# Kernel tuning notes

Measured on AMD Instinct MI355X. Metric: run time of the kernel, lower is better.

Reference implementation:

```python
import jax, jax.numpy as jnp
import numpy as np

EPS = 1e-5
S_CENTERS = 1024  # npoint//4
NSAMPLE = 32


def index_points(pts, idx):
    # pts [B,N,C], idx [B,...] int -> [B,...,C]
    return jax.vmap(lambda p, i: p[i])(pts, idx)


def farthest_point_sample(xyz, npoint):
    # xyz [B,N,3] -> [B,npoint] indices (deterministic start at index 0)
    B, N, _ = xyz.shape
    def body(carry, _):
        dist, far = carry
        centroid = jnp.take_along_axis(xyz, far[:, None, None], axis=1)  # [B,1,3]
        d = jnp.sum((xyz - centroid) ** 2, axis=-1)                      # [B,N]
        dist = jnp.minimum(dist, d)
        nxt = jnp.argmax(dist, axis=-1).astype(jnp.int32)
        return (dist, nxt), far
    init = (jnp.full((B, N), 1e10, xyz.dtype), jnp.zeros((B,), jnp.int32))
    _, idx = jax.lax.scan(body, init, None, length=npoint)
    return jnp.transpose(idx)  # [B,npoint]


def knn_point(k, xyz, new_xyz):
    # squared dists [B,S,N], take k nearest
    d = (jnp.sum(new_xyz ** 2, -1)[:, :, None]
         + jnp.sum(xyz ** 2, -1)[:, None, :]
         - 2.0 * jnp.einsum('bsc,bnc->bsn', new_xyz, xyz))
    _, idx = jax.lax.top_k(-d, k)
    return idx  # [B,S,k]


def instance_norm(h):
    # h [B,S,K,C]: InstanceNorm2d (affine=False) normalizes per (b,c) over spatial dims
    mu = jnp.mean(h, axis=(1, 2), keepdims=True)
    var = jnp.var(h, axis=(1, 2), keepdims=True)
    return (h - mu) * jax.lax.rsqrt(var + EPS)


def setup_inputs() -> dict:
    key = jax.random.key(0)
    ks = jax.random.split(key, 12)
    B, N, C = 8, 4096, 128
    inp = {
        'pc1_l_loc2': jax.random.normal(ks[0], (B, 3, N), jnp.float32),
        'corr_feats': jax.random.normal(ks[1], (B, C, N), jnp.float32),
        'W1': jax.random.normal(ks[2], (128, 131), jnp.float32) * 0.05,
        'b1': jnp.zeros((128,), jnp.float32),
        'W2': jax.random.normal(ks[3], (128, 128), jnp.float32) * 0.05,
        'b2': jnp.zeros((128,), jnp.float32),
        'W3': jax.random.normal(ks[4], (128, 128), jnp.float32) * 0.05,
        'b3': jnp.zeros((128,), jnp.float32),
        'fc_w': jax.random.normal(ks[5], (3, 128), jnp.float32) * 0.05,
        'fc_b': jnp.zeros((3,), jnp.float32),
    }
    return inp


def reference(pc1_l_loc2, corr_feats, W1, b1, W2, b2, W3, b3, fc_w, fc_b):
    xyz = jnp.transpose(pc1_l_loc2, (0, 2, 1))    # [B,N,3]
    points = jnp.transpose(corr_feats, (0, 2, 1))  # [B,N,128]

    fps_idx = farthest_point_sample(xyz, S_CENTERS)           # [B,S]
    new_xyz = index_points(xyz, fps_idx)                      # [B,S,3]
    idx = knn_point(NSAMPLE, xyz, new_xyz)                    # [B,S,K]
    grouped_xyz = index_points(xyz, idx)                      # [B,S,K,3]
    grouped_xyz_norm = grouped_xyz - new_xyz[:, :, None, :]
    grouped_pts = index_points(points, idx)                   # [B,S,K,128]
    h = jnp.concatenate([grouped_xyz_norm, grouped_pts], -1)  # [B,S,K,131]

    for W, b in ((W1, b1), (W2, b2), (W3, b3)):
        h = jnp.einsum('bskc,oc->bsko', h, W) + b  # 1x1 conv as matmul
        h = jax.nn.relu(instance_norm(h))

    x = jnp.max(h, axis=2)                         # [B,S,128] max over neighbors
    x = jnp.einsum('bsc,oc->bso', x, fc_w) + fc_b  # [B,S,3]
    flow0 = jnp.transpose(x, (0, 2, 1))            # [B,3,S]
    return flow0
```

## Files before the change

kernel.cpp:

```cpp
#include <hip/hip_runtime.h>
#include <hip/hip_fp16.h>

#define NB 8
#define NPTS 4096
#define NS 1024
#define NK 32
#define NM (NB*NS*NK)

typedef _Float16 f16x8 __attribute__((ext_vector_type(8)));
typedef float    f32x4 __attribute__((ext_vector_type(4)));
typedef float    f32x2 __attribute__((ext_vector_type(2)));

__device__ __forceinline__ float bf2f(unsigned short u){ return __uint_as_float(((unsigned)u)<<16); }
__device__ __forceinline__ unsigned short f2bf(float f){
  unsigned u = __float_as_uint(f);
  u = u + 0x7fffu + ((u>>16)&1u);
  return (unsigned short)(u>>16);
}
__device__ __forceinline__ unsigned long long umax64(unsigned long long a, unsigned long long b){ return a>b?a:b; }

#define DPP_STEP_MAX(x, ctrl, rm) { \
  unsigned _t = (unsigned)__builtin_amdgcn_update_dpp((int)(x), (int)(x), (ctrl), (rm), 0xf, false); \
  (x) = ((x) > _t) ? (x) : _t; }

__device__ __forceinline__ unsigned wave_max_u32(unsigned x){
  DPP_STEP_MAX(x, 0x111, 0xf);
  DPP_STEP_MAX(x, 0x112, 0xf);
  DPP_STEP_MAX(x, 0x114, 0xf);
  DPP_STEP_MAX(x, 0x118, 0xf);
  DPP_STEP_MAX(x, 0x142, 0xa);
  DPP_STEP_MAX(x, 0x143, 0xc);
  return (unsigned)__builtin_amdgcn_readlane((int)x, 63);
}

__device__ __forceinline__ bool detect_f32(const unsigned short* __restrict__ u){
  int huge_=0, zero_=0;
  #pragma unroll
  for (int i=0;i<64;i++){
    unsigned short w = u[i];
    if ((w & 0x7fffu) == 0) { zero_++; continue; }
    float a = fabsf(bf2f(w));
    if (a > 1e6f || a < 1e-6f) huge_++;
  }
  return (huge_ >= 8) || (zero_ >= 24);
}
__device__ __forceinline__ float ldin(const void* p, size_t i, bool f32){
  if (f32) return ((const float*)p)[i];
  else     return bf2f(((const unsigned short*)p)[i]);
}

__global__ __launch_bounds__(256) void fps_fused(const void* __restrict__ pc1,
                                                 const void* __restrict__ feats,
                                                 int* __restrict__ fps_out,
                                                 _Float16* __restrict__ G,
                                                 float* __restrict__ statz){
  __shared__ __align__(16) char smem[65600];
  int t = threadIdx.x;
  const bool f32 = detect_f32((const unsigned short*)pc1);
  if (blockIdx.x < 8){
    float4* cp4 = (float4*)smem;
    unsigned long long (*part)[4] = (unsigned long long (*)[4])(smem + 65536);
    int b = blockIdx.x;
    const size_t base = (size_t)b*3*NPTS;
    for (int i=t;i<NPTS;i+=256){
      float4 v;
      v.x = ldin(pc1, base+i, f32);
      v.y = ldin(pc1, base+NPTS+i, f32);
      v.z = ldin(pc1, base+2*NPTS+i, f32);
      v.w = 0.f;
      cp4[i] = v;
    }
    __syncthreads();
    f32x2 px[8],py[8],pz[8],dist[8];
    #pragma unroll
    for (int j=0;j<8;j++){
      float4 a = cp4[t*16+2*j], c = cp4[t*16+2*j+1];
      px[j] = f32x2{a.x, c.x};
      py[j] = f32x2{a.y, c.y};
      pz[j] = f32x2{a.z, c.z};
      dist[j] = f32x2{1e10f, 1e10f};
    }
    int far = 0;
    int w = t>>6, lane = t&63;
    for (int it=0; it<NS; it++){
      if (t==0) fps_out[b*NS+it] = far;
      float4 cc = cp4[far];
      f32x2 vcx = f32x2{cc.x,cc.x}, vcy = f32x2{cc.y,cc.y}, vcz = f32x2{cc.z,cc.z};
      {
        #pragma clang fp contract(off)
        #pragma unroll
        for (int j=0;j<8;j++){
          f32x2 dx = px[j]-vcx, dy = py[j]-vcy, dz = pz[j]-vcz;
          f32x2 d  = (dx*dx + dy*dy) + dz*dz;
          dist[j]  = __builtin_elementwise_min(dist[j], d);
        }
      }
      float d_[16];
      #pragma unroll
      for (int j=0;j<8;j++){ d_[2*j]=dist[j][0]; d_[2*j+1]=dist[j][1]; }
      float a0 = fmaxf(fmaxf(d_[0],d_[1]),d_[2]);
      float a1 = fmaxf(fmaxf(d_[3],d_[4]),d_[5]);
      float a2 = fmaxf(fmaxf(d_[6],d_[7]),d_[8]);
      float a3 = fmaxf(fmaxf(d_[9],d_[10]),d_[11]);
      float a4 = fmaxf(fmaxf(d_[12],d_[13]),d_[14]);
      float b0 = fmaxf(fmaxf(a0,a1),a2);
      float b1 = fmaxf(fmaxf(a3,a4),d_[15]);
      float bl = fmaxf(b0,b1);
      int li = 0;
      #pragma unroll
      for (int i=15;i>=0;i--) if (d_[i]==bl) li = i;
      unsigned blu = __float_as_uint(bl);
      unsigned wm = wave_max_u32(blu);
      unsigned long long mk = __ballot(blu == wm);
      int l = __builtin_ctzll(mk);
      int idx = __builtin_amdgcn_readlane(t*16+li, l);
      if (lane==0) part[it&1][w] = ((unsigned long long)wm<<32) | (unsigned)(NPTS-1-idx);
      __syncthreads();
      const ulonglong2* pp = (const ulonglong2*)&part[it&1][0];
      ulonglong2 A = pp[0], B = pp[1];
      unsigned long long m = umax64(umax64(A.x,A.y), umax64(B.x,B.y));
      far = NPTS-1 - (int)(m & 0xffffffffu);
    }
  } else {
    float (*tile)[65] = (float (*)[65])smem;
    int blk = blockIdx.x - 8;
    int b = blk>>6, n0 = (blk&63)*64;
    if (blk==0){
      for (int i=t;i<6144;i+=256) statz[i]=0.f;
    }
    #pragma unroll 4
    for (int i=0;i<32;i++){
      int idx = i*256 + t;
      int c = idx>>6, n = idx&63;
      tile[c][n] = ldin(feats, ((size_t)b*128 + c)*NPTS + n0 + n, f32);
    }
    __syncthreads();
    #pragma unroll 4
    for (int i=0;i<32;i++){
      int idx = i*256 + t;
      int n = idx>>7, c = idx&127;
      G[((size_t)b*NPTS + n0 + n)*136 + 3 + c] = (_Float16)tile[c][n];
    }
    if (t<64){
      size_t gb = ((size_t)b*NPTS + n0 + t)*136;
      G[gb]=(_Float16)0.f; G[gb+1]=(_Float16)0.f; G[gb+2]=(_Float16)0.f;
      #pragma unroll
      for (int c=131;c<136;c++) G[gb+c]=(_Float16)0.f;
    }
  }
}

__global__ __launch_bounds__(256) void knn_kernel(const void* __restrict__ pc1,
                                                  const int* __restrict__ fps_idx,
                                                  float* __restrict__ new_xyz,
                                                  int* __restrict__ knn_idx){
  __shared__ __align__(16) unsigned hist[4096];
  __shared__ __align__(16) unsigned long long cand[512];
  __shared__ unsigned part[256];
  __shared__ unsigned sup[16];
  __shared__ unsigned scal[2];
  int blk = blockIdx.x;
  int b = blk >> 10;
  int t = threadIdx.x;
  const bool f32 = detect_f32((const unsigned short*)pc1);
  const size_t base = (size_t)b*3*NPTS;
  int n0 = fps_idx[blk];
  float qx = ldin(pc1, base+n0, f32);
  float qy = ldin(pc1, base+NPTS+n0, f32);
  float qz = ldin(pc1, base+2*NPTS+n0, f32);
  if (t==0){
    new_xyz[(size_t)blk*3]=qx; new_xyz[(size_t)blk*3+1]=qy; new_xyz[(size_t)blk*3+2]=qz;
    scal[0]=0u;
  }
  #pragma unroll
  for (int j=0;j<16;j++) hist[j*256 + t] = 0u;
  float qn = __fadd_rn(__fadd_rn(__fmul_rn(qx,qx),__fmul_rn(qy,qy)),__fmul_rn(qz,qz));
  unsigned dv[16];
  #pragma unroll
  for (int k=0;k<16;k++){
    int n = t + 256*k;
    float x = ldin(pc1, base+n, f32);
    float y = ldin(pc1, base+NPTS+n, f32);
    float z = ldin(pc1, base+2*NPTS+n, f32);
    float pn = __fadd_rn(__fadd_rn(__fmul_rn(x,x),__fmul_rn(y,y)),__fmul_rn(z,z));
    float dt = __fadd_rn(__fadd_rn(__fmul_rn(qx,x),__fmul_rn(qy,y)),__fmul_rn(qz,z));
    float d  = __fsub_rn(__fadd_rn(qn,pn), __fmul_rn(2.f,dt));
    unsigned u = __float_as_uint(d);
    dv[k] = (u & 0x80000000u) ? ~u : (u | 0x80000000u);
  }
  __syncthreads();
  #pragma unroll
  for (int k=0;k<16;k++)
    atomicAdd(&hist[dv[k]>>20], 1u);
  __syncthreads();
  {
    unsigned s = 0;
    const uint4* hp = (const uint4*)&hist[t*16];
    #pragma unroll
    for (int j=0;j<4;j++){
      uint4 v = hp[j];
      s += v.x + v.y + v.z + v.w;
    }
    part[t] = s;
  }
  __syncthreads();
  if (t < 16){
    unsigned q = 0;
    #pragma unroll
    for (int j=0;j<16;j++) q += part[t*16 + j];
    sup[t] = q;
  }
  __syncthreads();
  if (t == 0){
    unsigned acc = 0; int sb = 0;
    for (; sb < 16; sb++){ unsigned v = sup[sb]; if (acc + v >= NK) break; acc += v; }
    int pt = sb*16;
    for (; pt < sb*16+16; pt++){ unsigned v = part[pt]; if (acc + v >= NK) break; acc += v; }
    int bn = pt*16;
    for (; bn < pt*16+16; bn++){ unsigned v = hist[bn]; if (acc + v >= NK) break; acc += v; }
    scal[1] = (unsigned)bn;
  }
  __syncthreads();
  unsigned beta = scal[1];
  #pragma unroll
  for (int k=0;k<16;k++){
    if ((dv[k]>>20) <= beta){
      unsigned pos = atomicAdd(&scal[0], 1u);
      if (pos < 512u)
        cand[pos] = ((unsigned long long)dv[k]<<32) | (unsigned)(t + 256*k);
    }
  }
  __syncthreads();
  int C = (int)scal[0]; if (C > 512) C = 512;
  for (int tt = t; tt < C; tt += 256){
    unsigned long long K = cand[tt];
    int rank = 0;
    for (int j = 0; j < C; j++) rank += (cand[j] < K) ? 1 : 0;
    if (rank < NK) knn_idx[(size_t)blk*NK + rank] = (int)(K & 0xffffffffu);
  }
}

template<int LAYER>
__global__ __launch_bounds__(256)
__attribute__((amdgpu_waves_per_eu(1,3)))
void conv_mfma(
    const void* __restrict__ pc1,
    const _Float16* __restrict__ G,
    const int* __restrict__ knn_idx,
    const float* __restrict__ new_xyz,
    const _Float16* __restrict__ Hin,
    const float* __restrict__ gp1,
    const float* __restrict__ gp2,
    const void* __restrict__ W,
    _Float16* __restrict__ Hout,
    float* __restrict__ gs1, float* __restrict__ gs2)
{
  constexpr int KC  = (LAYER==1)?131:128;
  constexpr int KCP = (LAYER==1)?160:128;
  constexpr int HSW = (LAYER==1)?168:136;
  __shared__ __align__(16) _Float16 hs[128][HSW];
  __shared__ __align__(16) _Float16 wt[(LAYER==1)?128:1][40];
  __shared__ float red1[4][64], red2[4][64];
  __shared__ int   nidx[128];
  __shared__ float cxyz[4][3];
  __shared__ __align__(16) _Float16 smuh[128], srsh[128];
  int blk = blockIdx.x;
  int m0 = blk*128;
  int b  = m0 >> 15;
  int t  = threadIdx.x;
  const bool f32 = detect_f32((const unsigned short*)pc1);
  int w = t>>6, lane = t&63;
  int l16 = lane&15, q = lane>>4, q8 = q*8;
  int wr = (w&1)*64, wc = (w>>1)*64;

  if (LAYER==1){
    if (t<128) nidx[t] = knn_idx[m0+t];
    if (t<12)  cxyz[t/3][t%3] = new_xyz[(size_t)(m0>>5)*3 + t];
    __syncthreads();
    for (int u=t; u<128*17; u+=256){
      int p = u/17, qq = u - p*17;
      const f16x8* src = (const f16x8*)(G + ((size_t)b*NPTS + nidx[p])*136 + qq*8);
      *(f16x8*)&hs[p][qq*8] = *src;
    }
    for (int u=t; u<128*3; u+=256){
      int p = u/3, qq = u - p*3;
      uint4 z; z.x=z.y=z.z=z.w=0u;
      *(uint4*)&hs[p][136+qq*8] = z;
    }
    __syncthreads();
    if (t<128){
      int n = nidx[t];
      float cx = cxyz[t>>5][0], cy = cxyz[t>>5][1], cz = cxyz[t>>5][2];
      hs[t][0] = (_Float16)(ldin(pc1, ((size_t)b*3+0)*NPTS+n, f32) - cx);
      hs[t][1] = (_Float16)(ldin(pc1, ((size_t)b*3+1)*NPTS+n, f32) - cy);
      hs[t][2] = (_Float16)(ldin(pc1, ((size_t)b*3+2)*NPTS+n, f32) - cz);
    }
    __syncthreads();
  } else {
    if (t<128){
      const float inv = 1.0f/32768.0f;
      float m = gp1[b*128+t]*inv;
      smuh[t] = (_Float16)m;
      srsh[t] = (_Float16)rsqrtf(gp2[b*128+t]*inv - m*m + 1e-5f);
    }
    __syncthreads();
    int p = t & 127, hi = t>>7;
    const _Float16* src = Hin + (size_t)(m0+p)*128 + hi*64;
    f16x8 zero8 = {};
    #pragma unroll
    for (int j=0;j<8;j++){
      f16x8 v   = *(const f16x8*)(src + j*8);
      f16x8 mu8 = *(const f16x8*)&smuh[hi*64 + j*8];
      f16x8 rs8 = *(const f16x8*)&srsh[hi*64 + j*8];
      f16x8 o = (v - mu8) * rs8;
      o = __builtin_elementwise_max(o, zero8);
      *(f16x8*)&hs[p][hi*64 + j*8] = o;
    }
    __syncthreads();
  }

  f32x4 acc[4][4];
  #pragma unroll
  for (int i=0;i<4;i++)
    #pragma unroll
    for (int c=0;c<4;c++){ acc[i][c][0]=0.f; acc[i][c][1]=0.f; acc[i][c][2]=0.f; acc[i][c][3]=0.f; }

  if (LAYER==1){
    for (int k0=0; k0<KCP; k0+=32){
      {
        int o = t>>1, half = t&1;
        f16x8 w0, w1;
        #pragma unroll
        for (int jj=0;jj<8;jj++){
          int c0 = k0 + half*16 + jj, c1 = c0 + 8;
          w0[jj] = (_Float16)((c0<KC) ? ldin(W, (size_t)o*KC + c0, f32) : 0.f);
          w1[jj] = (_Float16)((c1<KC) ? ldin(W, (size_t)o*KC + c1, f32) : 0.f);
        }
        *(f16x8*)&wt[o][half*16]     = w0;
        *(f16x8*)&wt[o][half*16 + 8] = w1;
      }
      __syncthreads();
      f16x8 av[4], bv[4];
      #pragma unroll
      for (int i=0;i<4;i++) av[i] = *(const f16x8*)&hs[wr + i*16 + l16][k0 + q8];
      #pragma unroll
      for (int c=0;c<4;c++) bv[c] = *(const f16x8*)&wt[wc + c*16 + l16][q8];
      #pragma unroll
      for (int i=0;i<4;i++)
        #pragma unroll
        for (int c=0;c<4;c++)
          acc[i][c] = __builtin_amdgcn_mfma_f32_16x16x32_f16(av[i], bv[c], acc[i][c], 0,0,0);
      __syncthreads();
    }
  } else {
    #pragma unroll
    for (int k0=0; k0<128; k0+=32){
      f16x8 av[4], bv[4];
      #pragma unroll
      for (int i=0;i<4;i++) av[i] = *(const f16x8*)&hs[wr + i*16 + l16][k0 + q8];
      #pragma unroll
      for (int c=0;c<4;c++){
        int row = wc + c*16 + l16;
        if (f32){
          const f32x4* Wr = (const f32x4*)((const float*)W + (size_t)row*128 + k0 + q8);
          f32x4 v0 = Wr[0], v1 = Wr[1];
          f16x8 bb;
          bb[0]=(_Float16)v0[0]; bb[1]=(_Float16)v0[1]; bb[2]=(_Float16)v0[2]; bb[3]=(_Float16)v0[3];
          bb[4]=(_Float16)v1[0]; bb[5]=(_Float16)v1[1]; bb[6]=(_Float16)v1[2]; bb[7]=(_Float16)v1[3];
          bv[c] = bb;
        } else {
          const ushort4* Wr = (const ushort4*)((const unsigned short*)W + (size_t)row*128 + k0 + q8);
          ushort4 u0 = Wr[0], u1 = Wr[1];
          f16x8 bb;
          bb[0]=(_Float16)bf2f(u0.x); bb[1]=(_Float16)bf2f(u0.y); bb[2]=(_Float16)bf2f(u0.z); bb[3]=(_Float16)bf2f(u0.w);
          bb[4]=(_Float16)bf2f(u1.x); bb[5]=(_Float16)bf2f(u1.y); bb[6]=(_Float16)bf2f(u1.z); bb[7]=(_Float16)bf2f(u1.w);
          bv[c] = bb;
        }
      }
      #pragma unroll
      for (int i=0;i<4;i++)
        #pragma unroll
        for (int c=0;c<4;c++)
          acc[i][c] = __builtin_amdgcn_mfma_f32_16x16x32_f16(av[i], bv[c], acc[i][c], 0,0,0);
    }
    __syncthreads();
  }

  #pragma unroll
  for (int c=0;c<4;c++){
    int o = wc + c*16 + l16;
    float s1=0.f, s2=0.f;
    #pragma unroll
    for (int i=0;i<4;i++){
      int row = wr + i*16 + q*4;
      #pragma unroll
      for (int r=0;r<4;r++){
        float v = acc[i][c][r];
        hs[row + r][o] = (_Float16)v;
        s1 += v; s2 = fmaf(v,v,s2);
      }
    }
    s1 += __shfl_xor(s1, 16, 64); s1 += __shfl_xor(s1, 32, 64);
    s2 += __shfl_xor(s2, 16, 64); s2 += __shfl_xor(s2, 32, 64);
    if (q==0){ red1[w][c*16+l16] = s1; red2[w][c*16+l16] = s2; }
  }
  __syncthreads();
  _Float16* dst0 = Hout + (size_t)m0*128;
  #pragma unroll
  for (int j=0;j<8;j++){
    int fi = j*256 + t;
    int row = fi >> 4, col = (fi & 15)*8;
    *(f16x8*)(dst0 + (size_t)fi*8) = *(const f16x8*)&hs[row][col];
  }
  if (t<128){
    int lo = t & 63, g = (t>>6)*2;
    unsafeAtomicAdd(&gs1[b*128+t], red1[g][lo] + red1[g+1][lo]);
    unsafeAtomicAdd(&gs2[b*128+t], red2[g][lo] + red2[g+1][lo]);
  }
}

__global__ __launch_bounds__(128) void final_kernel(
    const void* __restrict__ pc1,
    const _Float16* __restrict__ H,
    const float* __restrict__ gp1, const float* __restrict__ gp2,
    const void* __restrict__ fc_w, const void* __restrict__ fc_b,
    void* __restrict__ outv)
{
  __shared__ __align__(16) _Float16 tile[32][136];
  __shared__ float mv[128];
  int blk = blockIdx.x;
  int b = blk>>10, s = blk & 1023;
  int o = threadIdx.x;
  const bool f32 = detect_f32((const unsigned short*)pc1);
  const _Float16* src = H + (size_t)blk*NK*128;
  #pragma unroll
  for (int j=0;j<4;j++){
    int fi = j*128 + o;
    int row = fi >> 4, col = (fi & 15)*8;
    *(f16x8*)&tile[row][col] = *(const f16x8*)(src + (size_t)fi*8);
  }
  __syncthreads();
  int bo = b*128 + o;
  const float inv = 1.0f/32768.0f;
  float mu_ = gp1[bo]*inv;
  float rs_ = rsqrtf(gp2[bo]*inv - mu_*mu_ + 1e-5f);
  float m = -1e30f;
  #pragma unroll 4
  for (int k=0;k<NK;k++){
    float v = ((float)tile[k][o] - mu_)*rs_;
    m = fmaxf(m, v);
  }
  m = fmaxf(m, 0.f);
  mv[o] = m;
  __syncthreads();
  if (o<3){
    float acc = ldin(fc_b, o, f32);
    for(int c=0;c<128;c++) acc = fmaf(ldin(fc_w, (size_t)o*128+c, f32), mv[c], acc);
    size_t oi = ((size_t)b*3 + o)*NS + s;
    if (f32) ((float*)outv)[oi] = acc;
    else     ((unsigned short*)outv)[oi] = f2bf(acc);
  }
}

extern "C" void kernel_launch(void* const* d_in, const int* in_sizes, int n_in,
                              void* d_out, int out_size, void* d_ws, size_t ws_size,
                              hipStream_t stream){
  const void* pc1   = d_in[0];
  const void* feats = d_in[1];
  const void* W1    = d_in[2];
  const void* W2    = d_in[4];
  const void* W3    = d_in[6];
  const void* fcw   = d_in[8];
  const void* fcb   = d_in[9];
  char* ws = (char*)d_ws;
  int*      fps  = (int*)     (ws + 0);
  float*    nxyz = (float*)   (ws + 32768);
  int*      knn  = (int*)     (ws + 131072);
  float*    st   = (float*)   (ws + 1179648);
  _Float16* Ha   = (_Float16*)(ws + 1204224);
  _Float16* Hb   = (_Float16*)(ws + 68313088);
  _Float16* G    = Hb;

  fps_fused<<<8 + NB*64, 256, 0, stream>>>(pc1, feats, fps, G, st);
  knn_kernel<<<NB*NS, 256, 0, stream>>>(pc1, fps, nxyz, knn);

  conv_mfma<1><<<NM/128, 256, 0, stream>>>(pc1, G, knn, nxyz,
      (const _Float16*)nullptr, (const float*)nullptr, (const float*)nullptr,
      W1, Ha, st, st+1024);
  conv_mfma<2><<<NM/128, 256, 0, stream>>>(pc1, G, knn, nxyz,
      Ha, st, st+1024, W2, Hb, st+2048, st+3072);
  conv_mfma<3><<<NM/128, 256, 0, stream>>>(pc1, G, knn, nxyz,
      Hb, st+2048, st+3072, W3, Ha, st+4096, st+5120);

  final_kernel<<<NB*NS, 128, 0, stream>>>(pc1, Ha, st+4096, st+5120, fcw, fcb, d_out);
}
```

Baseline: 1.051 ms.

## Fuse KNN into FPS kernel with persistent workers polling FPS progress

Merges the KNN kernel into the FPS kernel. 504 persistent worker blocks first do the feature transpose, then process KNN queries in iteration order, spin-waiting on per-index FPS outputs that are published via relaxed atomic stores after a memset to -1. The FPS blocks get raised wave priority. This overlaps the long serial FPS loop with KNN work and removes a kernel boundary. The risks are a deadlock if the worker blocks are not co-resident with the FPS blocks, and ordering problems from relaxed-only atomics, plus the cost of the extra memset.

Result: faster. 950.2 us (-9.5%).

```diff
diff --git a/kernel.cpp b/kernel.cpp
--- a/kernel.cpp
+++ b/kernel.cpp
@@ -6,6 +6,7 @@
 #define NS 1024
 #define NK 32
 #define NM (NB*NS*NK)
+#define NWORK 504
 
 typedef _Float16 f16x8 __attribute__((ext_vector_type(8)));
 typedef float    f32x4 __attribute__((ext_vector_type(4)));
@@ -49,15 +50,20 @@
   else     return bf2f(((const unsigned short*)p)[i]);
 }
 
-__global__ __launch_bounds__(256) void fps_fused(const void* __restrict__ pc1,
-                                                 const void* __restrict__ feats,
-                                                 int* __restrict__ fps_out,
-                                                 _Float16* __restrict__ G,
-                                                 float* __restrict__ statz){
+__global__ __launch_bounds__(256, 2) void fps_knn_fused(
+    const void* __restrict__ pc1,
+    const void* __restrict__ feats,
+    int* __restrict__ fps_out,
+    _Float16* __restrict__ G,
+    float* __restrict__ statz,
+    float* __restrict__ new_xyz,
+    int* __restrict__ knn_idx)
+{
   __shared__ __align__(16) char smem[65600];
   int t = threadIdx.x;
   const bool f32 = detect_f32((const unsigned short*)pc1);
   if (blockIdx.x < 8){
+    __builtin_amdgcn_s_setprio(1);
     float4* cp4 = (float4*)smem;
     unsigned long long (*part)[4] = (unsigned long long (*)[4])(smem + 65536);
     int b = blockIdx.x;
@@ -83,7 +89,8 @@
     int far = 0;
     int w = t>>6, lane = t&63;
     for (int it=0; it<NS; it++){
-      if (t==0) fps_out[b*NS+it] = far;
+      if (t==0)
+        __hip_atomic_store(&fps_out[b*NS+it], far, __ATOMIC_RELAXED, __HIP_MEMORY_SCOPE_AGENT);
       float4 cc = cp4[far];
       f32x2 vcx = f32x2{cc.x,cc.x}, vcy = f32x2{cc.y,cc.y}, vcz = f32x2{cc.z,cc.z};
       {
@@ -122,121 +129,131 @@
       far = NPTS-1 - (int)(m & 0xffffffffu);
     }
   } else {
-    float (*tile)[65] = (float (*)[65])smem;
-    int blk = blockIdx.x - 8;
-    int b = blk>>6, n0 = (blk&63)*64;
-    if (blk==0){
-      for (int i=t;i<6144;i+=256) statz[i]=0.f;
-    }
-    #pragma unroll 4
-    for (int i=0;i<32;i++){
-      int idx = i*256 + t;
-      int c = idx>>6, n = idx&63;
-      tile[c][n] = ldin(feats, ((size_t)b*128 + c)*NPTS + n0 + n, f32);
-    }
-    __syncthreads();
-    #pragma unroll 4
-    for (int i=0;i<32;i++){
-      int idx = i*256 + t;
-      int n = idx>>7, c = idx&127;
-      G[((size_t)b*NPTS + n0 + n)*136 + 3 + c] = (_Float16)tile[c][n];
-    }
-    if (t<64){
-      size_t gb = ((size_t)b*NPTS + n0 + t)*136;
-      G[gb]=(_Float16)0.f; G[gb+1]=(_Float16)0.f; G[gb+2]=(_Float16)0.f;
-      #pragma unroll
-      for (int c=131;c<136;c++) G[gb+c]=(_Float16)0.f;
-    }
-  }
-}
-
-__global__ __launch_bounds__(256) void knn_kernel(const void* __restrict__ pc1,
-                                                  const int* __restrict__ fps_idx,
-                                                  float* __restrict__ new_xyz,
-                                                  int* __restrict__ knn_idx){
-  __shared__ __align__(16) unsigned hist[4096];
-  __shared__ __align__(16) unsigned long long cand[512];
-  __shared__ unsigned part[256];
-  __shared__ unsigned sup[16];
-  __shared__ unsigned scal[2];
-  int blk = blockIdx.x;
-  int b = blk >> 10;
-  int t = threadIdx.x;
-  const bool f32 = detect_f32((const unsigned short*)pc1);
-  const size_t base = (size_t)b*3*NPTS;
-  int n0 = fps_idx[blk];
-  float qx = ldin(pc1, base+n0, f32);
-  float qy = ldin(pc1, base+NPTS+n0, f32);
-  float qz = ldin(pc1, base+2*NPTS+n0, f32);
-  if (t==0){
-    new_xyz[(size_t)blk*3]=qx; new_xyz[(size_t)blk*3+1]=qy; new_xyz[(size_t)blk*3+2]=qz;
-    scal[0]=0u;
-  }
-  #pragma unroll
-  for (int j=0;j<16;j++) hist[j*256 + t] = 0u;
-  float qn = __fadd_rn(__fadd_rn(__fmul_rn(qx,qx),__fmul_rn(qy,qy)),__fmul_rn(qz,qz));
-  unsigned dv[16];
-  #pragma unroll
-  for (int k=0;k<16;k++){
-    int n = t + 256*k;
-    float x = ldin(pc1, base+n, f32);
-    float y = ldin(pc1, base+NPTS+n, f32);
-    float z = ldin(pc1, base+2*NPTS+n, f32);
-    float pn = __fadd_rn(__fadd_rn(__fmul_rn(x,x),__fmul_rn(y,y)),__fmul_rn(z,z));
-    float dt = __fadd_rn(__fadd_rn(__fmul_rn(qx,x),__fmul_rn(qy,y)),__fmul_rn(qz,z));
-    float d  = __fsub_rn(__fadd_rn(qn,pn), __fmul_rn(2.f,dt));
-    unsigned u = __float_as_uint(d);
-    dv[k] = (u & 0x80000000u) ? ~u : (u | 0x80000000u);
-  }
-  __syncthreads();
-  #pragma unroll
-  for (int k=0;k<16;k++)
-    atomicAdd(&hist[dv[k]>>20], 1u);
-  __syncthreads();
-  {
-    unsigned s = 0;
-    const uint4* hp = (const uint4*)&hist[t*16];
-    #pragma unroll
-    for (int j=0;j<4;j++){
-      uint4 v = hp[j];
-      s += v.x + v.y + v.z + v.w;
-    }
-    part[t] = s;
-  }
-  __syncthreads();
-  if (t < 16){
-    unsigned q = 0;
-    #pragma unroll
-    for (int j=0;j<16;j++) q += part[t*16 + j];
-    sup[t] = q;
-  }
-  __syncthreads();
-  if (t == 0){
-    unsigned acc = 0; int sb = 0;
-    for (; sb < 16; sb++){ unsigned v = sup[sb]; if (acc + v >= NK) break; acc += v; }
-    int pt = sb*16;
-    for (; pt < sb*16+16; pt++){ unsigned v = part[pt]; if (acc + v >= NK) break; acc += v; }
-    int bn = pt*16;
-    for (; bn < pt*16+16; bn++){ unsigned v = hist[bn]; if (acc + v >= NK) break; acc += v; }
-    scal[1] = (unsigned)bn;
-  }
-  __syncthreads();
-  unsigned beta = scal[1];
-  #pragma unroll
-  for (int k=0;k<16;k++){
-    if ((dv[k]>>20) <= beta){
-      unsigned pos = atomicAdd(&scal[0], 1u);
-      if (pos < 512u)
-        cand[pos] = ((unsigned long long)dv[k]<<32) | (unsigned)(t + 256*k);
-    }
-  }
-  __syncthreads();
-  int C = (int)scal[0]; if (C > 512) C = 512;
-  for (int tt = t; tt < C; tt += 256){
-    unsigned long long K = cand[tt];
-    int rank = 0;
-    for (int j = 0; j < C; j++) rank += (cand[j] < K) ? 1 : 0;
-    if (rank < NK) knn_idx[(size_t)blk*NK + rank] = (int)(K & 0xffffffffu);
+    int wid = blockIdx.x - 8;
+    {
+      float (*tile)[65] = (float (*)[65])smem;
+      if (wid==0){
+        for (int i=t;i<6144;i+=256) statz[i]=0.f;
+      }
+      for (int b2 = wid; b2 < 512; b2 += NWORK){
+        int b = b2>>6, n0 = (b2&63)*64;
+        #pragma unroll 4
+        for (int i=0;i<32;i++){
+          int idx = i*256 + t;
+          int c = idx>>6, n = idx&63;
+          tile[c][n] = ldin(feats, ((size_t)b*128 + c)*NPTS + n0 + n, f32);
+        }
+        __syncthreads();
+        #pragma unroll 4
+        for (int i=0;i<32;i++){
+          int idx = i*256 + t;
+          int n = idx>>7, c = idx&127;
+          G[((size_t)b*NPTS + n0 + n)*136 + 3 + c] = (_Float16)tile[c][n];
+        }
+        if (t<64){
+          size_t gb = ((size_t)b*NPTS + n0 + t)*136;
+          G[gb]=(_Float16)0.f; G[gb+1]=(_Float16)0.f; G[gb+2]=(_Float16)0.f;
+          #pragma unroll
+          for (int c=131;c<136;c++) G[gb+c]=(_Float16)0.f;
+        }
+        __syncthreads();
+      }
+    }
+    __syncthreads();
+    unsigned* hist            = (unsigned*)smem;
+    unsigned long long* cand  = (unsigned long long*)(smem + 16384);
+    unsigned* partk           = (unsigned*)(smem + 20480);
+    unsigned* sup             = (unsigned*)(smem + 21504);
+    unsigned* scal            = (unsigned*)(smem + 21568);
+    int* sn0                  = (int*)(smem + 21576);
+    for (int ci = wid; ci < NB*NS; ci += NWORK){
+      int b = ci & 7, s = ci >> 3;
+      int blk = (b<<10) | s;
+      if (t==0){
+        int nv;
+        while ((nv = __hip_atomic_load(&fps_out[b*NS+s], __ATOMIC_RELAXED,
+                                       __HIP_MEMORY_SCOPE_AGENT)) == -1)
+          __builtin_amdgcn_s_sleep(16);
+        *sn0 = nv;
+      }
+      __syncthreads();
+      const size_t base = (size_t)b*3*NPTS;
+      int n0 = *sn0;
+      float qx = ldin(pc1, base+n0, f32);
+      float qy = ldin(pc1, base+NPTS+n0, f32);
+      float qz = ldin(pc1, base+2*NPTS+n0, f32);
+      if (t==0){
+        new_xyz[(size_t)blk*3]=qx; new_xyz[(size_t)blk*3+1]=qy; new_xyz[(size_t)blk*3+2]=qz;
+        scal[0]=0u;
+      }
+      #pragma unroll
+      for (int j=0;j<16;j++) hist[j*256 + t] = 0u;
+      float qn = __fadd_rn(__fadd_rn(__fmul_rn(qx,qx),__fmul_rn(qy,qy)),__fmul_rn(qz,qz));
+      unsigned dv[16];
+      #pragma unroll
+      for (int k=0;k<16;k++){
+        int n = t + 256*k;
+        float x = ldin(pc1, base+n, f32);
+        float y = ldin(pc1, base+NPTS+n, f32);
+        float z = ldin(pc1, base+2*NPTS+n, f32);
+        float pn = __fadd_rn(__fadd_rn(__fmul_rn(x,x),__fmul_rn(y,y)),__fmul_rn(z,z));
+        float dt = __fadd_rn(__fadd_rn(__fmul_rn(qx,x),__fmul_rn(qy,y)),__fmul_rn(qz,z));
+        float d  = __fsub_rn(__fadd_rn(qn,pn), __fmul_rn(2.f,dt));
+        unsigned u = __float_as_uint(d);
+        dv[k] = (u & 0x80000000u) ? ~u : (u | 0x80000000u);
+      }
+      __syncthreads();
+      #pragma unroll
+      for (int k=0;k<16;k++)
+        atomicAdd(&hist[dv[k]>>20], 1u);
+      __syncthreads();
+      {
+        unsigned ssum = 0;
+        const uint4* hp = (const uint4*)&hist[t*16];
+        #pragma unroll
+        for (int j=0;j<4;j++){
+          uint4 v = hp[j];
+          ssum += v.x + v.y + v.z + v.w;
+        }
+        partk[t] = ssum;
+      }
+      __syncthreads();
+      if (t < 16){
+        unsigned qq = 0;
+        #pragma unroll
+        for (int j=0;j<16;j++) qq += partk[t*16 + j];
+        sup[t] = qq;
+      }
+      __syncthreads();
+      if (t == 0){
+        unsigned acc = 0; int sb = 0;
+        for (; sb < 16; sb++){ unsigned v = sup[sb]; if (acc + v >= NK) break; acc += v; }
+        int pt = sb*16;
+        for (; pt < sb*16+16; pt++){ unsigned v = partk[pt]; if (acc + v >= NK) break; acc += v; }
+        int bn = pt*16;
+        for (; bn < pt*16+16; bn++){ unsigned v = hist[bn]; if (acc + v >= NK) break; acc += v; }
+        scal[1] = (unsigned)bn;
+      }
+      __syncthreads();
+      unsigned beta = scal[1];
+      #pragma unroll
+      for (int k=0;k<16;k++){
+        if ((dv[k]>>20) <= beta){
+          unsigned pos = atomicAdd(&scal[0], 1u);
+          if (pos < 512u)
+            cand[pos] = ((unsigned long long)dv[k]<<32) | (unsigned)(t + 256*k);
+        }
+      }
+      __syncthreads();
+      int C = (int)scal[0]; if (C > 512) C = 512;
+      for (int tt = t; tt < C; tt += 256){
+        unsigned long long K = cand[tt];
+        int rank = 0;
+        for (int j = 0; j < C; j++) rank += (cand[j] < K) ? 1 : 0;
+        if (rank < NK) knn_idx[(size_t)blk*NK + rank] = (int)(K & 0xffffffffu);
+      }
+      __syncthreads();
+    }
   }
 }
 
@@ -481,8 +498,9 @@
   _Float16* Hb   = (_Float16*)(ws + 68313088);
   _Float16* G    = Hb;
 
-  fps_fused<<<8 + NB*64, 256, 0, stream>>>(pc1, feats, fps, G, st);
-  knn_kernel<<<NB*NS, 256, 0, stream>>>(pc1, fps, nxyz, knn);
+  hipMemsetAsync(fps, 0xFF, NB*NS*sizeof(int), stream);
+
+  fps_knn_fused<<<8 + NWORK, 256, 0, stream>>>(pc1, feats, fps, G, st, nxyz, knn);
 
   conv_mfma<1><<<NM/128, 256, 0, stream>>>(pc1, G, knn, nxyz,
       (const _Float16*)nullptr, (const float*)nullptr, (const float*)nullptr,
```
